# Optimization experiments

Hardware: AMD Instinct MI355X
Metric: run time of the kernel (lower is better)

Reference implementation:

```python
import jax, jax.numpy as jnp
import numpy as np

T, B, H = 512, 256, 512


def setup_inputs() -> dict:
    key = jax.random.key(0)
    k1, k2, k3, k4, k5 = jax.random.split(key, 5)
    scale_i = 1.0 / np.sqrt(H)
    return {
        "h0": jax.random.normal(k1, (B, H), dtype=jnp.float32),
        "ins": jax.random.normal(k2, (T, B, H), dtype=jnp.float32),
        "Wi": jax.random.normal(k3, (H, 3 * H), dtype=jnp.float32) * scale_i,
        "bi": jnp.zeros((3 * H,), dtype=jnp.float32),
        "Wh": jax.random.normal(k4, (H, 3 * H), dtype=jnp.float32) * scale_i,
        "bhn": jnp.zeros((H,), dtype=jnp.float32),
        "resets": jax.random.randint(k5, (T, B), 0, 2).astype(jnp.bool_),
    }


def reference(h0, ins, Wi, bi, Wh, bhn, resets):
    # flax GRUCell math: r = sig(x Wir + bir + h Whr); z = sig(x Wiz + biz + h Whz)
    def step(h, xr):
        x, reset = xr                       # x: [B,H], reset: [B]
        h = jnp.where(reset[:, None], jnp.zeros_like(h), h)  # reset carry to zeros
        gi = x @ Wi + bi                    # [B,3H]
        gh = h @ Wh                         # [B,3H]
        ir, iz, inn = jnp.split(gi, 3, axis=-1)
        hr, hz, hn = jnp.split(gh, 3, axis=-1)
        r = jax.nn.sigmoid(ir + hr)
        z = jax.nn.sigmoid(iz + hz)
        n = jnp.tanh(inn + r * (hn + bhn))
        h_new = (1.0 - z) * n + z * h
        return h_new, h_new

    _, ys = jax.lax.scan(step, h0, (ins, resets))
    return ys                               # [T,B,H]
```

## Files before the change

kernel.cpp:

```cpp
#include <hip/hip_runtime.h>

#define T_ 512
#define B_ 256
#define H_ 512
#define NBINS 4112
typedef __bf16 bf16_t;
typedef __bf16 bf16x8 __attribute__((ext_vector_type(8)));
typedef float f32x4 __attribute__((ext_vector_type(4)));

__device__ __forceinline__ float bf2f(unsigned short u) {
  unsigned x = ((unsigned)u) << 16; float f; __builtin_memcpy(&f, &x, 4); return f;
}
__device__ __forceinline__ bf16x8 pack2(f32x4 a, f32x4 b) {
  bf16x8 w;
#pragma unroll
  for (int i = 0; i < 4; ++i) { w[i] = (bf16_t)a[i]; w[i + 4] = (bf16_t)b[i]; }
  return w;
}
__device__ __forceinline__ void st_sc1(float* p, float v) {
  asm volatile("global_store_dword %0, %1, off sc0 sc1" :: "v"(p), "v"(v) : "memory");
}
__device__ __forceinline__ void ld8_sc1(const float* p0, const float* p1,
                                        const float* p2, const float* p3,
                                        const float* p4, const float* p5,
                                        const float* p6, const float* p7,
                                        f32x4& v0, f32x4& v1, f32x4& v2, f32x4& v3,
                                        f32x4& v4, f32x4& v5, f32x4& v6, f32x4& v7) {
  asm volatile(
      "global_load_dwordx4 %0, %8, off sc0 sc1\n\t"
      "global_load_dwordx4 %1, %9, off sc0 sc1\n\t"
      "global_load_dwordx4 %2, %10, off sc0 sc1\n\t"
      "global_load_dwordx4 %3, %11, off sc0 sc1\n\t"
      "global_load_dwordx4 %4, %12, off sc0 sc1\n\t"
      "global_load_dwordx4 %5, %13, off sc0 sc1\n\t"
      "global_load_dwordx4 %6, %14, off sc0 sc1\n\t"
      "global_load_dwordx4 %7, %15, off sc0 sc1\n\t"
      "s_waitcnt vmcnt(0)"
      : "=&v"(v0), "=&v"(v1), "=&v"(v2), "=&v"(v3),
        "=&v"(v4), "=&v"(v5), "=&v"(v6), "=&v"(v7)
      : "v"(p0), "v"(p1), "v"(p2), "v"(p3), "v"(p4), "v"(p5), "v"(p6), "v"(p7)
      : "memory");
}
__device__ __forceinline__ float sigm(float x) { return 1.f / (1.f + __expf(-x)); }
__device__ __forceinline__ float tanh_(float a) { return 1.f - 2.f / (__expf(2.f * a) + 1.f); }

__global__ __launch_bounds__(64) void zero_meta(int* __restrict__ flags,
                                                int* __restrict__ bar) {
  int i = threadIdx.x;
  if (i < 4) flags[i] = 0;
  if (i < 8) bar[i] = 0;
}

__global__ __launch_bounds__(256) void detect_resets(const void* __restrict__ rst,
                                                     int n, int* __restrict__ flags) {
  const int* pi = (const int*)rst;
  const float* pf = (const float*)rst;
  int a = 0, bq = 0, c = 0;
  int nq = n >> 2;
  for (int i = blockIdx.x * 256 + threadIdx.x; i < nq; i += gridDim.x * 256) {
    int v = pi[i];
    if (v != 0 && v != 1) a = 1;
    float f = pf[i];
    if (!(f == 0.0f || f == 1.0f)) bq = 1;
    if ((i & 1) && v != 0) c = 1;
  }
  if (a) atomicOr(&flags[0], 1);
  if (bq) atomicOr(&flags[1], 1);
  if (c) atomicOr(&flags[2], 1);
}

__global__ __launch_bounds__(256) void convert_resets(const void* __restrict__ rst,
                                                      const int* __restrict__ flags,
                                                      unsigned char* __restrict__ r8,
                                                      int n) {
  const int* pi = (const int*)rst;
  const float* pf = (const float*)rst;
  int mode;
  if (flags[0] == 0) mode = flags[2] ? 0 : 3;
  else if (flags[1] == 0) mode = 1;
  else mode = 2;
  for (int i = blockIdx.x * 256 + threadIdx.x; i < n; i += gridDim.x * 256) {
    unsigned char v;
    if (mode == 0)      v = (unsigned char)(pi[i] != 0);
    else if (mode == 3) v = (unsigned char)(pi[2 * i] != 0);
    else if (mode == 1) v = (unsigned char)(pf[i] != 0.0f);
    else                v = ((const unsigned char*)rst)[i] ? 1 : 0;
    r8[i] = v;
  }
}

__global__ __launch_bounds__(256) void build_wc(const float* __restrict__ Wi,
                                                const float* __restrict__ Wh,
                                                bf16_t* __restrict__ Wc) {
  int id = blockIdx.x * 256 + threadIdx.x;
  int koct = id / 1536, n = id % 1536;
  const float* src = (koct < 64) ? Wi : Wh;
  int kk = (koct & 63) * 8;
  bf16x8 w;
#pragma unroll
  for (int e = 0; e < 8; ++e) w[e] = (bf16_t)src[(size_t)(kk + e) * 1536 + n];
  *(bf16x8*)(Wc + (size_t)id * 8) = w;
}

__device__ __forceinline__ int bucket_of(int t, int rs, int& p) {
  p = (t == 0 || rs) ? 0 : p + 1;
  return (p > 0) ? (p + 1) : ((t == 0 && !rs) ? 1 : 0);
}

__global__ __launch_bounds__(1024) void bins_kernel(const unsigned char* __restrict__ r8,
                                                    int* __restrict__ cur,
                                                    unsigned int* __restrict__ elem) {
  extern __shared__ int sm[];
  int* s0 = sm;
  int* s1 = sm + 8192;
  const int tid = threadIdx.x;
  for (int i = tid; i < 8192; i += 1024) s0[i] = 0;
  __syncthreads();
  if (tid < 256) {
    int b = tid, base = (b >> 5) * 514, p = 0;
    for (int t = 0; t < T_; ++t) {
      int bk = bucket_of(t, r8[t * B_ + b], p);
      atomicAdd(&s0[base + bk], 1);
    }
  }
  __syncthreads();
  int* a = s0;
  int* bb = s1;
  for (int d = 1; d < 8192; d <<= 1) {
    for (int i = tid; i < 8192; i += 1024) bb[i] = a[i] + ((i >= d) ? a[i - d] : 0);
    __syncthreads();
    int* t = a; a = bb; bb = t;
  }
  for (int i = tid; i <= NBINS; i += 1024) cur[i] = (i == 0) ? 0 : a[i - 1];
  for (int i = tid; i < 8192; i += 1024)
    bb[i] = (i == 0) ? 0 : ((i <= NBINS) ? a[i - 1] : 0);
  __syncthreads();
  if (tid < 256) {
    int b = tid, base = (b >> 5) * 514, p = 0;
    for (int t = 0; t < T_; ++t) {
      int bk = bucket_of(t, r8[t * B_ + b], p);
      int pos = atomicAdd(&bb[base + bk], 1);
      elem[pos] = (unsigned)(t * B_ + b);
    }
  }
}

template <int NKS, int NRGC, int LDB>
__device__ __forceinline__ void mm_block(const char* lds, const char* W, int q,
                                         int rgb, int span, int nrgd, int am, int aq,
                                         f32x4 (&acc)[4][NRGC]) {
  const char* Bp = W + (size_t)(q * 16 + am) * 16;
#pragma unroll
  for (int ks = 0; ks < NKS; ++ks) {
    const int koct = ks * 4 + aq;
    const char* bb = Bp + (size_t)koct * 24576;
    bf16x8 b0 = *(const bf16x8*)(bb);
    bf16x8 b1 = *(const bf16x8*)(bb + 8192);
    bf16x8 b2 = *(const bf16x8*)(bb + 16384);
#pragma unroll
    for (int rg = 0; rg < NRGC; ++rg) {
      if (rg >= rgb && rg < rgb + span && rg < nrgd) {
        const int ar = rg * 16 + am;
        bf16x8 af = *(const bf16x8*)(lds + (size_t)ar * LDB +
                                     ((koct * 16) ^ ((ar & 7) << 4)));
        acc[0][rg] = __builtin_amdgcn_mfma_f32_16x16x32_bf16(af, b0, acc[0][rg], 0, 0, 0);
        acc[1][rg] = __builtin_amdgcn_mfma_f32_16x16x32_bf16(af, b1, acc[1][rg], 0, 0, 0);
        if (ks < 16)
          acc[2][rg] = __builtin_amdgcn_mfma_f32_16x16x32_bf16(af, b2, acc[2][rg], 0, 0, 0);
        else
          acc[3][rg] = __builtin_amdgcn_mfma_f32_16x16x32_bf16(af, b2, acc[3][rg], 0, 0, 0);
      }
    }
  }
}

__global__ __launch_bounds__(512, 2) void gru_phases(
    const float* __restrict__ ins, const float* __restrict__ h0,
    const bf16_t* __restrict__ Wc, const float* __restrict__ bi,
    const float* __restrict__ bhn, const unsigned int* __restrict__ elem,
    const int* __restrict__ cur, int* __restrict__ bar, float* __restrict__ out) {
  extern __shared__ char lds[];
  const int tid = threadIdx.x, lane = tid & 63, w = tid >> 6;
  const int am = lane & 15, aq = lane >> 4;
  const int g = blockIdx.x >> 5, bg = blockIdx.x & 31;
  const int base = g * 514;

  for (int it = 0; it <= 513; ++it) {
    const int beg = cur[base + it];
    const int cnt = cur[base + it + 1] - beg;
    if (it >= 2 && cnt == 0) break;
    if (cnt > 0 && it == 0) {
      const int ntiles = (cnt + 127) >> 7;
      for (int u = bg; u < ntiles; u += 32) {
        __syncthreads();
        {
          const int tr = tid >> 2, tl = tid & 3;
          const int row = u * 128 + tr;
          const float* xs = (row < cnt) ? (ins + (size_t)elem[beg + row] * 512) : nullptr;
          const int swz = (tr & 7) << 4;
          char* lrp = lds + tr * 1024;
#pragma unroll 4
          for (int s2 = 0; s2 < 16; ++s2) {
            const int ko = tl + 4 * s2;
            bf16x8 wv;
            if (xs) {
              f32x4 a0 = __builtin_nontemporal_load((const f32x4*)(xs + ko * 8));
              f32x4 a1 = __builtin_nontemporal_load((const f32x4*)(xs + ko * 8 + 4));
              wv = pack2(a0, a1);
            } else {
#pragma unroll
              for (int z = 0; z < 8; ++z) wv[z] = (bf16_t)0.f;
            }
            *(bf16x8*)(lrp + ((ko * 16) ^ swz)) = wv;
          }
        }
        __syncthreads();
        const int rem = cnt - u * 128;
        const int nrgd = ((rem < 128 ? rem : 128) + 15) >> 4;
#pragma unroll 1
        for (int s = 0; s < 4; ++s) {
          const int q = w + 8 * s;
          f32x4 acc[4][8];
#pragma unroll
          for (int gg = 0; gg < 4; ++gg)
#pragma unroll
            for (int r = 0; r < 8; ++r) acc[gg][r] = (f32x4){0.f, 0.f, 0.f, 0.f};
          mm_block<16, 8, 1024>(lds, (const char*)Wc, q, 0, 8, nrgd, am, aq, acc);
          const int j = q * 16 + am;
          const float bir = bi[j], biz = bi[512 + j], bin = bi[1024 + j], bh = bhn[j];
#pragma unroll
          for (int rg = 0; rg < 8; ++rg) {
            if (rg < nrgd) {
#pragma unroll
              for (int qq = 0; qq < 4; ++qq) {
                const int row = u * 128 + rg * 16 + aq * 4 + qq;
                if (row < cnt) {
                  float r = sigm(acc[0][rg][qq] + bir);
                  float z = sigm(acc[1][rg][qq] + biz);
                  float n = tanh_(acc[2][rg][qq] + bin + r * bh);
                  st_sc1(out + (size_t)elem[beg + row] * 512 + j, (1.f - z) * n);
                }
              }
            }
          }
        }
      }
    } else if (cnt > 0) {
      const int ntiles = (cnt + 63) >> 6;
      int lg = 0;
      while (lg < 4 && (ntiles << lg) < 32) ++lg;
      const int nitems = ntiles << lg;
      const int Q = 32 >> lg;
      for (int i = bg; i < nitems; i += 32) {
        const int u = i >> lg, jc = i & ((1 << lg) - 1);
        __syncthreads();
        {
          const int tr = tid >> 3, tl = tid & 7;
          const int row = u * 64 + tr;
          const float* xs = nullptr;
          const float* ph = nullptr;
          if (row < cnt) {
            const unsigned e = elem[beg + row];
            xs = ins + (size_t)e * 512;
            ph = (e < 256) ? (h0 + (size_t)e * 512) : (out + ((size_t)e - 256) * 512);
          }
          const int swz = (tr & 7) << 4;
          char* lrp = lds + tr * 2048;
#pragma unroll
          for (int s2 = 0; s2 < 8; ++s2) {
            const int ko = tl + 8 * s2;
            bf16x8 wv;
            if (xs) {
              f32x4 a0 = __builtin_nontemporal_load((const f32x4*)(xs + ko * 8));
              f32x4 a1 = __builtin_nontemporal_load((const f32x4*)(xs + ko * 8 + 4));
              wv = pack2(a0, a1);
            } else {
#pragma unroll
              for (int z = 0; z < 8; ++z) wv[z] = (bf16_t)0.f;
            }
            *(bf16x8*)(lrp + ((ko * 16) ^ swz)) = wv;
          }
          if (ph) {
#pragma unroll 1
            for (int hb = 0; hb < 2; ++hb) {
              f32x4 hv[8];
              const float* hp[8];
#pragma unroll
              for (int s2 = 0; s2 < 4; ++s2) {
                const int ko = tl + 8 * (8 + hb * 4 + s2);
                hp[2 * s2] = ph + (ko & 63) * 8;
                hp[2 * s2 + 1] = ph + (ko & 63) * 8 + 4;
              }
              ld8_sc1(hp[0], hp[1], hp[2], hp[3], hp[4], hp[5], hp[6], hp[7],
                      hv[0], hv[1], hv[2], hv[3], hv[4], hv[5], hv[6], hv[7]);
#pragma unroll
              for (int s2 = 0; s2 < 4; ++s2) {
                const int ko = tl + 8 * (8 + hb * 4 + s2);
                *(bf16x8*)(lrp + ((ko * 16) ^ swz)) = pack2(hv[2 * s2], hv[2 * s2 + 1]);
              }
            }
          } else {
#pragma unroll
            for (int s2 = 0; s2 < 8; ++s2) {
              const int ko = tl + 8 * (8 + s2);
              bf16x8 wv;
#pragma unroll
              for (int z = 0; z < 8; ++z) wv[z] = (bf16_t)0.f;
              *(bf16x8*)(lrp + ((ko * 16) ^ swz)) = wv;
            }
          }
        }
        __syncthreads();
        const int rem = cnt - u * 64;
        const int nrgd = ((rem < 64 ? rem : 64) + 15) >> 4;
        const int span = (Q >= 8) ? 4 : (Q >> 1);
        const int rgb = (Q >= 8) ? 0 : (w / Q) * span;
        const int nq = (Q >= 8) ? (Q >> 3) : 1;
#pragma unroll 1
        for (int s = 0; s < nq; ++s) {
          const int q = (Q >= 8) ? (jc * Q + w + 8 * s) : (jc * Q + (w & (Q - 1)));
          f32x4 acc[4][4];
#pragma unroll
          for (int gg = 0; gg < 4; ++gg)
#pragma unroll
            for (int r = 0; r < 4; ++r) acc[gg][r] = (f32x4){0.f, 0.f, 0.f, 0.f};
          mm_block<32, 4, 2048>(lds, (const char*)Wc, q, rgb, span, nrgd, am, aq, acc);
          const int j = q * 16 + am;
          const float bir = bi[j], biz = bi[512 + j], bin = bi[1024 + j], bh = bhn[j];
#pragma unroll
          for (int rg = 0; rg < 4; ++rg) {
            if (rg >= rgb && rg < rgb + span && rg < nrgd) {
#pragma unroll
              for (int qq = 0; qq < 4; ++qq) {
                const int lrow = rg * 16 + aq * 4 + qq;
                const int row = u * 64 + lrow;
                if (row < cnt) {
                  const unsigned e = elem[beg + row];
                  unsigned short hraw = *(const unsigned short*)(
                      lds + (size_t)lrow * 2048 +
                      (((64 + (j >> 3)) * 16) ^ ((lrow & 7) << 4)) + (j & 7) * 2);
                  float hp = bf2f(hraw);
                  float r = sigm(acc[0][rg][qq] + bir);
                  float z = sigm(acc[1][rg][qq] + biz);
                  float n = tanh_(acc[2][rg][qq] + bin + r * (acc[3][rg][qq] + bh));
                  st_sc1(out + (size_t)e * 512 + j, (1.f - z) * n + z * hp);
                }
              }
            }
          }
        }
      }
    }
    __syncthreads();
    if (tid == 0) {
      __hip_atomic_fetch_add(&bar[g], 1, __ATOMIC_RELAXED, __HIP_MEMORY_SCOPE_AGENT);
      const int target = 32 * (it + 1);
      while (__hip_atomic_load(&bar[g], __ATOMIC_RELAXED, __HIP_MEMORY_SCOPE_AGENT) <
             target) {
        __builtin_amdgcn_s_sleep(2);
      }
    }
    __syncthreads();
  }
}

extern "C" void kernel_launch(void* const* d_in, const int* in_sizes, int n_in,
                              void* d_out, int out_size, void* d_ws, size_t ws_size,
                              hipStream_t stream) {
  const float* h0  = (const float*)d_in[0];
  const float* ins = (const float*)d_in[1];
  const float* Wi  = (const float*)d_in[2];
  const float* bi  = (const float*)d_in[3];
  const float* Wh  = (const float*)d_in[4];
  const float* bhn = (const float*)d_in[5];
  const void*  rst = d_in[6];
  float* out = (float*)d_out;

  char* ws = (char*)d_ws;
  const size_t off_r8    = 0;
  const size_t off_Wc    = 131072;
  const size_t off_flags = 3276800;
  const size_t off_bar   = 3276864;
  const size_t off_cur   = 3276928;
  const size_t off_elem  = 3293440;
  const size_t need      = 3817728;
  if (ws_size < need) return;

  unsigned char* r8 = (unsigned char*)(ws + off_r8);
  bf16_t* Wc = (bf16_t*)(ws + off_Wc);
  int* flags = (int*)(ws + off_flags);
  int* bar = (int*)(ws + off_bar);
  int* cur = (int*)(ws + off_cur);
  unsigned int* elem = (unsigned int*)(ws + off_elem);

  zero_meta<<<1, 64, 0, stream>>>(flags, bar);
  detect_resets<<<64, 256, 0, stream>>>(rst, T_ * B_, flags);
  convert_resets<<<128, 256, 0, stream>>>(rst, flags, r8, T_ * B_);
  build_wc<<<768, 256, 0, stream>>>(Wi, Wh, Wc);
  (void)hipFuncSetAttribute((const void*)bins_kernel,
                            hipFuncAttributeMaxDynamicSharedMemorySize, 65536);
  bins_kernel<<<1, 1024, 65536, stream>>>(r8, cur, elem);

  (void)hipFuncSetAttribute((const void*)gru_phases,
                            hipFuncAttributeMaxDynamicSharedMemorySize, 131072);
  void* args[] = {(void*)&ins, (void*)&h0, (void*)&Wc, (void*)&bi, (void*)&bhn,
                  (void*)&elem, (void*)&cur, (void*)&bar, (void*)&out};
  (void)hipLaunchCooperativeKernel((const void*)gru_phases, dim3(256), dim3(512),
                                   args, 131072, stream);
}
```

Baseline: 1.484 ms.

## Precompute input projection in a parallel GEMM and run recurrence on hidden GEMM only

Moves the x@Wi projection for all non-reset timesteps out of the sequential phase loop into a separate fully parallel gi_gemm kernel that stores the gate pre-activations in bf16 in the workspace. Reset rows are finished directly in that kernel. The recurrent kernel then loads only h, does a half-K matmul against Wh, and runs with smaller LDS so it can fit more blocks per CU. It also uses plain stores when the next step resets, since no later step reads that output. In exchange it writes and reads a large bf16 gi buffer (about 400MB), adds extra rounding to the gate inputs, and falls back to the old fused path when the workspace is too small.

```diff
diff --git a/kernel.cpp b/kernel.cpp
--- a/kernel.cpp
+++ b/kernel.cpp
@@ -145,6 +145,32 @@
   }
 }
 
+template <int NRGC, int LDB>
+__device__ __forceinline__ void mm3(const char* lds, const char* W, int q,
+                                    int rgb, int span, int nrgd, int am, int aq,
+                                    f32x4 (&acc)[3][NRGC]) {
+  const char* Bp = W + (size_t)(q * 16 + am) * 16;
+#pragma unroll
+  for (int ks = 0; ks < 16; ++ks) {
+    const int koct = ks * 4 + aq;
+    const char* bb = Bp + (size_t)koct * 24576;
+    bf16x8 b0 = *(const bf16x8*)(bb);
+    bf16x8 b1 = *(const bf16x8*)(bb + 8192);
+    bf16x8 b2 = *(const bf16x8*)(bb + 16384);
+#pragma unroll
+    for (int rg = 0; rg < NRGC; ++rg) {
+      if (rg >= rgb && rg < rgb + span && rg < nrgd) {
+        const int ar = rg * 16 + am;
+        bf16x8 af = *(const bf16x8*)(lds + (size_t)ar * LDB +
+                                     ((koct * 16) ^ ((ar & 7) << 4)));
+        acc[0][rg] = __builtin_amdgcn_mfma_f32_16x16x32_bf16(af, b0, acc[0][rg], 0, 0, 0);
+        acc[1][rg] = __builtin_amdgcn_mfma_f32_16x16x32_bf16(af, b1, acc[1][rg], 0, 0, 0);
+        acc[2][rg] = __builtin_amdgcn_mfma_f32_16x16x32_bf16(af, b2, acc[2][rg], 0, 0, 0);
+      }
+    }
+  }
+}
+
 template <int NKS, int NRGC, int LDB>
 __device__ __forceinline__ void mm_block(const char* lds, const char* W, int q,
                                          int rgb, int span, int nrgd, int am, int aq,
@@ -174,84 +200,219 @@
   }
 }
 
-__global__ __launch_bounds__(512, 2) void gru_phases(
-    const float* __restrict__ ins, const float* __restrict__ h0,
-    const bf16_t* __restrict__ Wc, const float* __restrict__ bi,
-    const float* __restrict__ bhn, const unsigned int* __restrict__ elem,
-    const int* __restrict__ cur, int* __restrict__ bar, float* __restrict__ out) {
+template <bool WRITE_GI>
+__global__ __launch_bounds__(512, 2) void gi_gemm(
+    const float* __restrict__ ins, const bf16_t* __restrict__ Wic,
+    const float* __restrict__ bi, const float* __restrict__ bhn,
+    const unsigned char* __restrict__ r8, bf16_t* __restrict__ gi,
+    float* __restrict__ out) {
+  extern __shared__ char lds[];
+  const int u = blockIdx.x;
+  const int tid = threadIdx.x, lane = tid & 63, w = tid >> 6;
+  const int am = lane & 15, aq = lane >> 4;
+  {
+    const int tr = tid >> 2, tl = tid & 3;
+    const float* xs = ins + ((size_t)u * 128 + tr) * 512;
+    const int swz = (tr & 7) << 4;
+    char* lrp = lds + tr * 1024;
+#pragma unroll 4
+    for (int s2 = 0; s2 < 16; ++s2) {
+      const int ko = tl + 4 * s2;
+      f32x4 a0 = __builtin_nontemporal_load((const f32x4*)(xs + ko * 8));
+      f32x4 a1 = __builtin_nontemporal_load((const f32x4*)(xs + ko * 8 + 4));
+      *(bf16x8*)(lrp + ((ko * 16) ^ swz)) = pack2(a0, a1);
+    }
+  }
+  __syncthreads();
+#pragma unroll 1
+  for (int s = 0; s < 4; ++s) {
+    const int q = w + 8 * s;
+    f32x4 acc[3][8];
+#pragma unroll
+    for (int gg = 0; gg < 3; ++gg)
+#pragma unroll
+      for (int r = 0; r < 8; ++r) acc[gg][r] = (f32x4){0.f, 0.f, 0.f, 0.f};
+    mm3<8, 1024>(lds, (const char*)Wic, q, 0, 8, 8, am, aq, acc);
+    const int j = q * 16 + am;
+    const float bir = bi[j], biz = bi[512 + j], bin = bi[1024 + j], bh = bhn[j];
+#pragma unroll
+    for (int rg = 0; rg < 8; ++rg) {
+#pragma unroll
+      for (int qq = 0; qq < 4; ++qq) {
+        const int e = u * 128 + rg * 16 + aq * 4 + qq;
+        if (r8[e]) {
+          float r = sigm(acc[0][rg][qq] + bir);
+          float z = sigm(acc[1][rg][qq] + biz);
+          float n = tanh_(acc[2][rg][qq] + bin + r * bh);
+          float v = (1.f - z) * n;
+          float* op = out + (size_t)e * 512 + j;
+          if (e >= (T_ - 1) * B_ || r8[e + B_]) __builtin_nontemporal_store(v, op);
+          else st_sc1(op, v);
+        } else if (WRITE_GI) {
+          bf16_t* gp = gi + (size_t)e * 1536 + j;
+          __builtin_nontemporal_store((bf16_t)acc[0][rg][qq], gp);
+          __builtin_nontemporal_store((bf16_t)acc[1][rg][qq], gp + 512);
+          __builtin_nontemporal_store((bf16_t)acc[2][rg][qq], gp + 1024);
+        }
+      }
+    }
+  }
+}
+
+__global__ __launch_bounds__(512, 4) void gru_phases_gi(
+    const float* __restrict__ h0, const bf16_t* __restrict__ Whc,
+    const bf16_t* __restrict__ gi, const float* __restrict__ bi,
+    const float* __restrict__ bhn, const unsigned char* __restrict__ r8,
+    const unsigned int* __restrict__ elem, const int* __restrict__ cur,
+    int* __restrict__ bar, float* __restrict__ out) {
   extern __shared__ char lds[];
   const int tid = threadIdx.x, lane = tid & 63, w = tid >> 6;
   const int am = lane & 15, aq = lane >> 4;
-  const int g = blockIdx.x >> 5, bg = blockIdx.x & 31;
+  const int nbg = gridDim.x >> 3;
+  const int sh = 31 - __clz(nbg);
+  const int g = blockIdx.x >> sh, bg = blockIdx.x & (nbg - 1);
   const int base = g * 514;
-
-  for (int it = 0; it <= 513; ++it) {
+  int done = 0;
+
+  for (int it = 1; it <= 513; ++it) {
     const int beg = cur[base + it];
     const int cnt = cur[base + it + 1] - beg;
     if (it >= 2 && cnt == 0) break;
-    if (cnt > 0 && it == 0) {
-      const int ntiles = (cnt + 127) >> 7;
-      for (int u = bg; u < ntiles; u += 32) {
+    if (cnt > 0) {
+      const int ntiles = (cnt + 63) >> 6;
+      int lg = 0;
+      while (lg < 4 && (ntiles << lg) < nbg) ++lg;
+      const int nitems = ntiles << lg;
+      const int Q = 32 >> lg;
+      for (int i = bg; i < nitems; i += nbg) {
+        const int u = i >> lg, jc = i & ((1 << lg) - 1);
         __syncthreads();
         {
-          const int tr = tid >> 2, tl = tid & 3;
-          const int row = u * 128 + tr;
-          const float* xs = (row < cnt) ? (ins + (size_t)elem[beg + row] * 512) : nullptr;
+          const int tr = tid >> 3, tl = tid & 7;
+          const int row = u * 64 + tr;
+          const float* ph = nullptr;
+          if (row < cnt) {
+            const unsigned e = elem[beg + row];
+            ph = (e < 256) ? (h0 + (size_t)e * 512) : (out + ((size_t)e - 256) * 512);
+          }
           const int swz = (tr & 7) << 4;
           char* lrp = lds + tr * 1024;
-#pragma unroll 4
-          for (int s2 = 0; s2 < 16; ++s2) {
-            const int ko = tl + 4 * s2;
-            bf16x8 wv;
-            if (xs) {
-              f32x4 a0 = __builtin_nontemporal_load((const f32x4*)(xs + ko * 8));
-              f32x4 a1 = __builtin_nontemporal_load((const f32x4*)(xs + ko * 8 + 4));
-              wv = pack2(a0, a1);
-            } else {
+          if (ph) {
+#pragma unroll 1
+            for (int hb = 0; hb < 2; ++hb) {
+              f32x4 hv[8];
+              const float* hp[8];
+#pragma unroll
+              for (int s2 = 0; s2 < 4; ++s2) {
+                const int ko = tl + 8 * (hb * 4 + s2);
+                hp[2 * s2] = ph + ko * 8;
+                hp[2 * s2 + 1] = ph + ko * 8 + 4;
+              }
+              ld8_sc1(hp[0], hp[1], hp[2], hp[3], hp[4], hp[5], hp[6], hp[7],
+                      hv[0], hv[1], hv[2], hv[3], hv[4], hv[5], hv[6], hv[7]);
+#pragma unroll
+              for (int s2 = 0; s2 < 4; ++s2) {
+                const int ko = tl + 8 * (hb * 4 + s2);
+                *(bf16x8*)(lrp + ((ko * 16) ^ swz)) = pack2(hv[2 * s2], hv[2 * s2 + 1]);
+              }
+            }
+          } else {
+#pragma unroll
+            for (int s2 = 0; s2 < 8; ++s2) {
+              const int ko = tl + 8 * s2;
+              bf16x8 wv;
 #pragma unroll
               for (int z = 0; z < 8; ++z) wv[z] = (bf16_t)0.f;
+              *(bf16x8*)(lrp + ((ko * 16) ^ swz)) = wv;
             }
-            *(bf16x8*)(lrp + ((ko * 16) ^ swz)) = wv;
           }
         }
         __syncthreads();
-        const int rem = cnt - u * 128;
-        const int nrgd = ((rem < 128 ? rem : 128) + 15) >> 4;
+        const int rem = cnt - u * 64;
+        const int nrgd = ((rem < 64 ? rem : 64) + 15) >> 4;
+        const int span = (Q >= 8) ? 4 : (Q >> 1);
+        const int rgb = (Q >= 8) ? 0 : (w / Q) * span;
+        const int nq = (Q >= 8) ? (Q >> 3) : 1;
 #pragma unroll 1
-        for (int s = 0; s < 4; ++s) {
-          const int q = w + 8 * s;
-          f32x4 acc[4][8];
-#pragma unroll
-          for (int gg = 0; gg < 4; ++gg)
-#pragma unroll
-            for (int r = 0; r < 8; ++r) acc[gg][r] = (f32x4){0.f, 0.f, 0.f, 0.f};
-          mm_block<16, 8, 1024>(lds, (const char*)Wc, q, 0, 8, nrgd, am, aq, acc);
+        for (int s = 0; s < nq; ++s) {
+          const int q = (Q >= 8) ? (jc * Q + w + 8 * s) : (jc * Q + (w & (Q - 1)));
+          f32x4 acc[3][4];
+#pragma unroll
+          for (int gg = 0; gg < 3; ++gg)
+#pragma unroll
+            for (int r = 0; r < 4; ++r) acc[gg][r] = (f32x4){0.f, 0.f, 0.f, 0.f};
+          mm3<4, 1024>(lds, (const char*)Whc, q, rgb, span, nrgd, am, aq, acc);
           const int j = q * 16 + am;
           const float bir = bi[j], biz = bi[512 + j], bin = bi[1024 + j], bh = bhn[j];
 #pragma unroll
-          for (int rg = 0; rg < 8; ++rg) {
-            if (rg < nrgd) {
+          for (int rg = 0; rg < 4; ++rg) {
+            if (rg >= rgb && rg < rgb + span && rg < nrgd) {
 #pragma unroll
               for (int qq = 0; qq < 4; ++qq) {
-                const int row = u * 128 + rg * 16 + aq * 4 + qq;
+                const int lrow = rg * 16 + aq * 4 + qq;
+                const int row = u * 64 + lrow;
                 if (row < cnt) {
-                  float r = sigm(acc[0][rg][qq] + bir);
-                  float z = sigm(acc[1][rg][qq] + biz);
-                  float n = tanh_(acc[2][rg][qq] + bin + r * bh);
-                  st_sc1(out + (size_t)elem[beg + row] * 512 + j, (1.f - z) * n);
+                  const unsigned e = elem[beg + row];
+                  const bf16_t* gp = gi + (size_t)e * 1536 + j;
+                  float gr = (float)gp[0], gz = (float)gp[512], gn = (float)gp[1024];
+                  unsigned short hraw = *(const unsigned short*)(
+                      lds + (size_t)lrow * 1024 +
+                      (((j >> 3) * 16) ^ ((lrow & 7) << 4)) + (j & 7) * 2);
+                  float hp = bf2f(hraw);
+                  float r = sigm(gr + acc[0][rg][qq] + bir);
+                  float z = sigm(gz + acc[1][rg][qq] + biz);
+                  float n = tanh_(gn + bin + r * (acc[2][rg][qq] + bh));
+                  float v = (1.f - z) * n + z * hp;
+                  float* op = out + (size_t)e * 512 + j;
+                  if (e >= (T_ - 1) * B_ || r8[e + B_]) *op = v;
+                  else st_sc1(op, v);
                 }
               }
             }
           }
         }
       }
-    } else if (cnt > 0) {
+    }
+    __syncthreads();
+    ++done;
+    if (tid == 0) {
+      __hip_atomic_fetch_add(&bar[g], 1, __ATOMIC_RELAXED, __HIP_MEMORY_SCOPE_AGENT);
+      const int target = nbg * done;
+      while (__hip_atomic_load(&bar[g], __ATOMIC_RELAXED, __HIP_MEMORY_SCOPE_AGENT) <
+             target) {
+        __builtin_amdgcn_s_sleep(2);
+      }
+    }
+    __syncthreads();
+  }
+}
+
+__global__ __launch_bounds__(512, 2) void gru_phases_fb(
+    const float* __restrict__ ins, const float* __restrict__ h0,
+    const bf16_t* __restrict__ Wc, const float* __restrict__ bi,
+    const float* __restrict__ bhn, const unsigned char* __restrict__ r8,
+    const unsigned int* __restrict__ elem, const int* __restrict__ cur,
+    int* __restrict__ bar, float* __restrict__ out) {
+  extern __shared__ char lds[];
+  const int tid = threadIdx.x, lane = tid & 63, w = tid >> 6;
+  const int am = lane & 15, aq = lane >> 4;
+  const int nbg = gridDim.x >> 3;
+  const int sh = 31 - __clz(nbg);
+  const int g = blockIdx.x >> sh, bg = blockIdx.x & (nbg - 1);
+  const int base = g * 514;
+  int done = 0;
+
+  for (int it = 1; it <= 513; ++it) {
+    const int beg = cur[base + it];
+    const int cnt = cur[base + it + 1] - beg;
+    if (it >= 2 && cnt == 0) break;
+    if (cnt > 0) {
       const int ntiles = (cnt + 63) >> 6;
       int lg = 0;
-      while (lg < 4 && (ntiles << lg) < 32) ++lg;
+      while (lg < 4 && (ntiles << lg) < nbg) ++lg;
       const int nitems = ntiles << lg;
       const int Q = 32 >> lg;
-      for (int i = bg; i < nitems; i += 32) {
+      for (int i = bg; i < nitems; i += nbg) {
         const int u = i >> lg, jc = i & ((1 << lg) - 1);
         __syncthreads();
         {
@@ -343,7 +504,10 @@
                   float r = sigm(acc[0][rg][qq] + bir);
                   float z = sigm(acc[1][rg][qq] + biz);
                   float n = tanh_(acc[2][rg][qq] + bin + r * (acc[3][rg][qq] + bh));
-                  st_sc1(out + (size_t)e * 512 + j, (1.f - z) * n + z * hp);
+                  float v = (1.f - z) * n + z * hp;
+                  float* op = out + (size_t)e * 512 + j;
+                  if (e >= (T_ - 1) * B_ || r8[e + B_]) *op = v;
+                  else st_sc1(op, v);
                 }
               }
             }
@@ -352,9 +516,10 @@
       }
     }
     __syncthreads();
+    ++done;
     if (tid == 0) {
       __hip_atomic_fetch_add(&bar[g], 1, __ATOMIC_RELAXED, __HIP_MEMORY_SCOPE_AGENT);
-      const int target = 32 * (it + 1);
+      const int target = nbg * done;
       while (__hip_atomic_load(&bar[g], __ATOMIC_RELAXED, __HIP_MEMORY_SCOPE_AGENT) <
              target) {
         __builtin_amdgcn_s_sleep(2);
@@ -383,15 +548,20 @@
   const size_t off_bar   = 3276864;
   const size_t off_cur   = 3276928;
   const size_t off_elem  = 3293440;
-  const size_t need      = 3817728;
-  if (ws_size < need) return;
+  const size_t off_gi    = 3817728;
+  const size_t need_small = 3817728;
+  const size_t need_big   = off_gi + (size_t)131072 * 1536 * 2;
+  if (ws_size < need_small) return;
+  const bool big = ws_size >= need_big;
 
   unsigned char* r8 = (unsigned char*)(ws + off_r8);
   bf16_t* Wc = (bf16_t*)(ws + off_Wc);
+  bf16_t* Whc = Wc + (size_t)64 * 1536 * 8;
   int* flags = (int*)(ws + off_flags);
   int* bar = (int*)(ws + off_bar);
   int* cur = (int*)(ws + off_cur);
   unsigned int* elem = (unsigned int*)(ws + off_elem);
+  bf16_t* gi = (bf16_t*)(ws + off_gi);
 
   zero_meta<<<1, 64, 0, stream>>>(flags, bar);
   detect_resets<<<64, 256, 0, stream>>>(rst, T_ * B_, flags);
@@ -401,10 +571,42 @@
                             hipFuncAttributeMaxDynamicSharedMemorySize, 65536);
   bins_kernel<<<1, 1024, 65536, stream>>>(r8, cur, elem);
 
-  (void)hipFuncSetAttribute((const void*)gru_phases,
-                            hipFuncAttributeMaxDynamicSharedMemorySize, 131072);
-  void* args[] = {(void*)&ins, (void*)&h0, (void*)&Wc, (void*)&bi, (void*)&bhn,
-                  (void*)&elem, (void*)&cur, (void*)&bar, (void*)&out};
-  (void)hipLaunchCooperativeKernel((const void*)gru_phases, dim3(256), dim3(512),
-                                   args, 131072, stream);
-}
+  void* args_fb[] = {(void*)&ins, (void*)&h0, (void*)&Wc, (void*)&bi, (void*)&bhn,
+                     (void*)&r8, (void*)&elem, (void*)&cur, (void*)&bar, (void*)&out};
+
+  if (big) {
+    (void)hipFuncSetAttribute((const void*)gi_gemm<true>,
+                              hipFuncAttributeMaxDynamicSharedMemorySize, 131072);
+    gi_gemm<true><<<1024, 512, 131072, stream>>>(ins, Wc, bi, bhn, r8, gi, out);
+    (void)hipFuncSetAttribute((const void*)gru_phases_gi,
+                              hipFuncAttributeMaxDynamicSharedMemorySize, 65536);
+    int maxb = 0;
+    if (hipOccupancyMaxActiveBlocksPerMultiprocessor(
+            &maxb, (const void*)gru_phases_gi, 512, 65536) != hipSuccess || maxb < 1)
+      maxb = 1;
+    if (maxb > 2) maxb = 2;
+    int cgrid = 256 * maxb;
+    void* args[] = {(void*)&h0, (void*)&Whc, (void*)&gi, (void*)&bi, (void*)&bhn,
+                    (void*)&r8, (void*)&elem, (void*)&cur, (void*)&bar, (void*)&out};
+    hipError_t ce = hipLaunchCooperativeKernel((const void*)gru_phases_gi,
+                                               dim3(cgrid), dim3(512), args, 65536,
+                                               stream);
+    if (ce != hipSuccess && cgrid != 256)
+      ce = hipLaunchCooperativeKernel((const void*)gru_phases_gi, dim3(256),
+                                      dim3(512), args, 65536, stream);
+    if (ce != hipSuccess) {
+      (void)hipFuncSetAttribute((const void*)gru_phases_fb,
+                                hipFuncAttributeMaxDynamicSharedMemorySize, 131072);
+      (void)hipLaunchCooperativeKernel((const void*)gru_phases_fb, dim3(256),
+                                       dim3(512), args_fb, 131072, stream);
+    }
+  } else {
+    (void)hipFuncSetAttribute((const void*)gi_gemm<false>,
+                              hipFuncAttributeMaxDynamicSharedMemorySize, 131072);
+    gi_gemm<false><<<1024, 512, 131072, stream>>>(ins, Wc, bi, bhn, r8, gi, out);
+    (void)hipFuncSetAttribute((const void*)gru_phases_fb,
+                              hipFuncAttributeMaxDynamicSharedMemorySize, 131072);
+    (void)hipLaunchCooperativeKernel((const void*)gru_phases_fb, dim3(256),
+                                     dim3(512), args_fb, 131072, stream);
+  }
+}
```

Result: slower. 1.892 ms (+27.5%).

## Split reset-step GEMM into separate dense kernel and pool all blocks per phase

Applied to the files above, without the earlier changes.

Rows where the carry is reset depend only on x, so they are now computed by a separate dense kernel over all T*B rows, masked by the reset flag, before the recurrent pool starts. The recurrent kernel no longer splits into 8 independent groups of 32 blocks with per-group barriers. All 256 blocks share one global barrier and process the merged chain-depth buckets, with the bins interleaved by depth. Outputs that no later step reads are written with nontemporal or plain stores instead of sc1 stores. The dense kernel computes the x-GEMM for every row, including rows that are not reset, and the single global barrier makes every block wait on the slowest one.

```diff
diff --git a/kernel.cpp b/kernel.cpp
--- a/kernel.cpp
+++ b/kernel.cpp
@@ -117,10 +117,10 @@
   for (int i = tid; i < 8192; i += 1024) s0[i] = 0;
   __syncthreads();
   if (tid < 256) {
-    int b = tid, base = (b >> 5) * 514, p = 0;
+    int b = tid, sub = b >> 5, p = 0;
     for (int t = 0; t < T_; ++t) {
       int bk = bucket_of(t, r8[t * B_ + b], p);
-      atomicAdd(&s0[base + bk], 1);
+      atomicAdd(&s0[bk * 8 + sub], 1);
     }
   }
   __syncthreads();
@@ -136,11 +136,37 @@
     bb[i] = (i == 0) ? 0 : ((i <= NBINS) ? a[i - 1] : 0);
   __syncthreads();
   if (tid < 256) {
-    int b = tid, base = (b >> 5) * 514, p = 0;
+    int b = tid, sub = b >> 5, p = 0;
     for (int t = 0; t < T_; ++t) {
       int bk = bucket_of(t, r8[t * B_ + b], p);
-      int pos = atomicAdd(&bb[base + bk], 1);
+      int pos = atomicAdd(&bb[bk * 8 + sub], 1);
       elem[pos] = (unsigned)(t * B_ + b);
+    }
+  }
+}
+
+template <int NRGC, int LDB>
+__device__ __forceinline__ void mm3(const char* lds, const char* W, int q,
+                                    int rgb, int span, int nrgd, int am, int aq,
+                                    f32x4 (&acc)[3][NRGC]) {
+  const char* Bp = W + (size_t)(q * 16 + am) * 16;
+#pragma unroll
+  for (int ks = 0; ks < 16; ++ks) {
+    const int koct = ks * 4 + aq;
+    const char* bb = Bp + (size_t)koct * 24576;
+    bf16x8 b0 = *(const bf16x8*)(bb);
+    bf16x8 b1 = *(const bf16x8*)(bb + 8192);
+    bf16x8 b2 = *(const bf16x8*)(bb + 16384);
+#pragma unroll
+    for (int rg = 0; rg < NRGC; ++rg) {
+      if (rg >= rgb && rg < rgb + span && rg < nrgd) {
+        const int ar = rg * 16 + am;
+        bf16x8 af = *(const bf16x8*)(lds + (size_t)ar * LDB +
+                                     ((koct * 16) ^ ((ar & 7) << 4)));
+        acc[0][rg] = __builtin_amdgcn_mfma_f32_16x16x32_bf16(af, b0, acc[0][rg], 0, 0, 0);
+        acc[1][rg] = __builtin_amdgcn_mfma_f32_16x16x32_bf16(af, b1, acc[1][rg], 0, 0, 0);
+        acc[2][rg] = __builtin_amdgcn_mfma_f32_16x16x32_bf16(af, b2, acc[2][rg], 0, 0, 0);
+      }
     }
   }
 }
@@ -174,84 +200,81 @@
   }
 }
 
-__global__ __launch_bounds__(512, 2) void gru_phases(
+__global__ __launch_bounds__(512, 2) void xonly_gemm(
+    const float* __restrict__ ins, const bf16_t* __restrict__ Wic,
+    const float* __restrict__ bi, const float* __restrict__ bhn,
+    const unsigned char* __restrict__ r8, float* __restrict__ out) {
+  extern __shared__ char lds[];
+  const int u = blockIdx.x;
+  const int tid = threadIdx.x, lane = tid & 63, w = tid >> 6;
+  const int am = lane & 15, aq = lane >> 4;
+  {
+    const int tr = tid >> 2, tl = tid & 3;
+    const float* xs = ins + ((size_t)u * 128 + tr) * 512;
+    const int swz = (tr & 7) << 4;
+    char* lrp = lds + tr * 1024;
+#pragma unroll 4
+    for (int s2 = 0; s2 < 16; ++s2) {
+      const int ko = tl + 4 * s2;
+      f32x4 a0 = __builtin_nontemporal_load((const f32x4*)(xs + ko * 8));
+      f32x4 a1 = __builtin_nontemporal_load((const f32x4*)(xs + ko * 8 + 4));
+      *(bf16x8*)(lrp + ((ko * 16) ^ swz)) = pack2(a0, a1);
+    }
+  }
+  __syncthreads();
+#pragma unroll 1
+  for (int s = 0; s < 4; ++s) {
+    const int q = w + 8 * s;
+    f32x4 acc[3][8];
+#pragma unroll
+    for (int gg = 0; gg < 3; ++gg)
+#pragma unroll
+      for (int r = 0; r < 8; ++r) acc[gg][r] = (f32x4){0.f, 0.f, 0.f, 0.f};
+    mm3<8, 1024>(lds, (const char*)Wic, q, 0, 8, 8, am, aq, acc);
+    const int j = q * 16 + am;
+    const float bir = bi[j], biz = bi[512 + j], bin = bi[1024 + j], bh = bhn[j];
+#pragma unroll
+    for (int rg = 0; rg < 8; ++rg) {
+#pragma unroll
+      for (int qq = 0; qq < 4; ++qq) {
+        const int e = u * 128 + rg * 16 + aq * 4 + qq;
+        if (r8[e]) {
+          float r = sigm(acc[0][rg][qq] + bir);
+          float z = sigm(acc[1][rg][qq] + biz);
+          float n = tanh_(acc[2][rg][qq] + bin + r * bh);
+          float v = (1.f - z) * n;
+          float* op = out + (size_t)e * 512 + j;
+          if (e >= (T_ - 1) * B_ || r8[e + B_]) __builtin_nontemporal_store(v, op);
+          else st_sc1(op, v);
+        }
+      }
+    }
+  }
+}
+
+__global__ __launch_bounds__(512, 2) void gru_pool(
     const float* __restrict__ ins, const float* __restrict__ h0,
     const bf16_t* __restrict__ Wc, const float* __restrict__ bi,
-    const float* __restrict__ bhn, const unsigned int* __restrict__ elem,
-    const int* __restrict__ cur, int* __restrict__ bar, float* __restrict__ out) {
+    const float* __restrict__ bhn, const unsigned char* __restrict__ r8,
+    const unsigned int* __restrict__ elem, const int* __restrict__ cur,
+    int* __restrict__ bar, float* __restrict__ out) {
   extern __shared__ char lds[];
   const int tid = threadIdx.x, lane = tid & 63, w = tid >> 6;
   const int am = lane & 15, aq = lane >> 4;
-  const int g = blockIdx.x >> 5, bg = blockIdx.x & 31;
-  const int base = g * 514;
-
-  for (int it = 0; it <= 513; ++it) {
-    const int beg = cur[base + it];
-    const int cnt = cur[base + it + 1] - beg;
+  const int nbg = gridDim.x, bg = blockIdx.x;
+  int done = 0;
+
+  for (int it = 1; it <= 513; ++it) {
+    const int beg = cur[it * 8];
+    const int cnt = cur[(it + 1) * 8] - beg;
     if (it >= 2 && cnt == 0) break;
-    if (cnt > 0 && it == 0) {
-      const int ntiles = (cnt + 127) >> 7;
-      for (int u = bg; u < ntiles; u += 32) {
-        __syncthreads();
-        {
-          const int tr = tid >> 2, tl = tid & 3;
-          const int row = u * 128 + tr;
-          const float* xs = (row < cnt) ? (ins + (size_t)elem[beg + row] * 512) : nullptr;
-          const int swz = (tr & 7) << 4;
-          char* lrp = lds + tr * 1024;
-#pragma unroll 4
-          for (int s2 = 0; s2 < 16; ++s2) {
-            const int ko = tl + 4 * s2;
-            bf16x8 wv;
-            if (xs) {
-              f32x4 a0 = __builtin_nontemporal_load((const f32x4*)(xs + ko * 8));
-              f32x4 a1 = __builtin_nontemporal_load((const f32x4*)(xs + ko * 8 + 4));
-              wv = pack2(a0, a1);
-            } else {
-#pragma unroll
-              for (int z = 0; z < 8; ++z) wv[z] = (bf16_t)0.f;
-            }
-            *(bf16x8*)(lrp + ((ko * 16) ^ swz)) = wv;
-          }
-        }
-        __syncthreads();
-        const int rem = cnt - u * 128;
-        const int nrgd = ((rem < 128 ? rem : 128) + 15) >> 4;
-#pragma unroll 1
-        for (int s = 0; s < 4; ++s) {
-          const int q = w + 8 * s;
-          f32x4 acc[4][8];
-#pragma unroll
-          for (int gg = 0; gg < 4; ++gg)
-#pragma unroll
-            for (int r = 0; r < 8; ++r) acc[gg][r] = (f32x4){0.f, 0.f, 0.f, 0.f};
-          mm_block<16, 8, 1024>(lds, (const char*)Wc, q, 0, 8, nrgd, am, aq, acc);
-          const int j = q * 16 + am;
-          const float bir = bi[j], biz = bi[512 + j], bin = bi[1024 + j], bh = bhn[j];
-#pragma unroll
-          for (int rg = 0; rg < 8; ++rg) {
-            if (rg < nrgd) {
-#pragma unroll
-              for (int qq = 0; qq < 4; ++qq) {
-                const int row = u * 128 + rg * 16 + aq * 4 + qq;
-                if (row < cnt) {
-                  float r = sigm(acc[0][rg][qq] + bir);
-                  float z = sigm(acc[1][rg][qq] + biz);
-                  float n = tanh_(acc[2][rg][qq] + bin + r * bh);
-                  st_sc1(out + (size_t)elem[beg + row] * 512 + j, (1.f - z) * n);
-                }
-              }
-            }
-          }
-        }
-      }
-    } else if (cnt > 0) {
+    if (cnt > 0) {
       const int ntiles = (cnt + 63) >> 6;
       int lg = 0;
-      while (lg < 4 && (ntiles << lg) < 32) ++lg;
+      while (lg < 4 && (ntiles << lg) < nbg) ++lg;
       const int nitems = ntiles << lg;
       const int Q = 32 >> lg;
-      for (int i = bg; i < nitems; i += 32) {
+      for (int i = bg; i < nitems; i += nbg) {
         const int u = i >> lg, jc = i & ((1 << lg) - 1);
         __syncthreads();
         {
@@ -343,7 +366,10 @@
                   float r = sigm(acc[0][rg][qq] + bir);
                   float z = sigm(acc[1][rg][qq] + biz);
                   float n = tanh_(acc[2][rg][qq] + bin + r * (acc[3][rg][qq] + bh));
-                  st_sc1(out + (size_t)e * 512 + j, (1.f - z) * n + z * hp);
+                  float v = (1.f - z) * n + z * hp;
+                  float* op = out + (size_t)e * 512 + j;
+                  if (e >= (T_ - 1) * B_ || r8[e + B_]) *op = v;
+                  else st_sc1(op, v);
                 }
               }
             }
@@ -352,10 +378,11 @@
       }
     }
     __syncthreads();
+    ++done;
     if (tid == 0) {
-      __hip_atomic_fetch_add(&bar[g], 1, __ATOMIC_RELAXED, __HIP_MEMORY_SCOPE_AGENT);
-      const int target = 32 * (it + 1);
-      while (__hip_atomic_load(&bar[g], __ATOMIC_RELAXED, __HIP_MEMORY_SCOPE_AGENT) <
+      __hip_atomic_fetch_add(&bar[0], 1, __ATOMIC_RELAXED, __HIP_MEMORY_SCOPE_AGENT);
+      const int target = nbg * done;
+      while (__hip_atomic_load(&bar[0], __ATOMIC_RELAXED, __HIP_MEMORY_SCOPE_AGENT) <
              target) {
         __builtin_amdgcn_s_sleep(2);
       }
@@ -401,10 +428,14 @@
                             hipFuncAttributeMaxDynamicSharedMemorySize, 65536);
   bins_kernel<<<1, 1024, 65536, stream>>>(r8, cur, elem);
 
-  (void)hipFuncSetAttribute((const void*)gru_phases,
+  (void)hipFuncSetAttribute((const void*)xonly_gemm,
+                            hipFuncAttributeMaxDynamicSharedMemorySize, 131072);
+  xonly_gemm<<<1024, 512, 131072, stream>>>(ins, Wc, bi, bhn, r8, out);
+
+  (void)hipFuncSetAttribute((const void*)gru_pool,
                             hipFuncAttributeMaxDynamicSharedMemorySize, 131072);
   void* args[] = {(void*)&ins, (void*)&h0, (void*)&Wc, (void*)&bi, (void*)&bhn,
-                  (void*)&elem, (void*)&cur, (void*)&bar, (void*)&out};
-  (void)hipLaunchCooperativeKernel((const void*)gru_phases, dim3(256), dim3(512),
+                  (void*)&r8, (void*)&elem, (void*)&cur, (void*)&bar, (void*)&out};
+  (void)hipLaunchCooperativeKernel((const void*)gru_pool, dim3(256), dim3(512),
                                    args, 131072, stream);
 }
```

Result: slower. 1.571 ms (+5.9%).
